# Kernel tuning notes

Measured on AMD Instinct MI355X. Metric: run time of the kernel, lower is better.

The kernel has to match this reference:

```python
import jax, jax.numpy as jnp
import numpy as np

B, P, D = 64, 128, 128   # clouds, points per cloud, vec_dim
N = B * P                # 8192 nodes
EPS = 1e-5


def _complete_graph_edges():
    # knn_graph with k == total node count => complete graph per cloud (no self loops)
    i = np.arange(P)
    ii, jj = np.meshgrid(i, i, indexing='ij')
    m = ii != jj
    li, lj = ii[m], jj[m]                      # [P*(P-1)] local pairs
    off = (np.arange(B) * P)[:, None]          # cloud offsets
    src = (off + li[None, :]).reshape(-1)      # neighbor index
    dst = (off + lj[None, :]).reshape(-1)      # center index
    return jnp.asarray(src, jnp.int32), jnp.asarray(dst, jnp.int32)


def setup_inputs() -> dict:
    key = jax.random.key(0)
    ks = jax.random.split(key, 4)
    src, dst = _complete_graph_edges()
    return {
        'x': jax.random.normal(ks[0], (N, D), jnp.float32),
        'xyz': jax.random.normal(ks[1], (N, 3), jnp.float32),
        'W_xyz': jax.random.normal(ks[2], (3, D), jnp.float32) * 0.1,
        'bn_gamma': jnp.ones((D,), jnp.float32),
        'bn_beta': jnp.zeros((D,), jnp.float32),
        'W1': jax.random.normal(ks[3], (D, D), jnp.float32) * 0.05,
        'b1': jnp.zeros((D,), jnp.float32),
        'ln_gamma': jnp.ones((D,), jnp.float32),
        'ln_beta': jnp.zeros((D,), jnp.float32),
        'src': src,
        'dst': dst,
    }


def reference(x, xyz, W_xyz, bn_gamma, bn_beta, W1, b1, ln_gamma, ln_beta, src, dst):
    n = x.shape[0]
    rela_xyz = xyz[src] - xyz[dst]                         # [E, 3]
    rela_x = x[src] - x[dst]                               # [E, D]
    dist = jnp.sqrt(jnp.sum(rela_xyz * rela_xyz, axis=-1))  # [E]
    w = jnp.exp(-dist)[:, None]                            # [E, 1]

    # weighted linear + relu, pool by src (global_add_pool over node index)
    h1 = jax.nn.relu((w * rela_x) @ W1 + b1)               # [E, D]
    p1 = jax.ops.segment_sum(h1, src, num_segments=n)      # [N, D]
    mu = jnp.mean(p1, axis=-1, keepdims=True)
    var = jnp.var(p1, axis=-1, keepdims=True)
    x = x + ((p1 - mu) / jnp.sqrt(var + EPS)) * ln_gamma + ln_beta

    # xyz projection branch, BatchNorm1d (training-mode batch stats)
    h2 = jax.nn.relu(rela_xyz @ W_xyz)                     # [E, D]
    p2 = jax.ops.segment_sum(h2, src, num_segments=n)      # [N, D]
    bmu = jnp.mean(p2, axis=0)
    bvar = jnp.var(p2, axis=0)
    x = x + ((p2 - bmu) / jnp.sqrt(bvar + EPS)) * bn_gamma + bn_beta
    return x
```

## Files before the change

kernel.cpp:

```cpp
#include <hip/hip_runtime.h>
#include <stdint.h>

#define EPS 1e-5f
#define N_NODES 8192

typedef __attribute__((ext_vector_type(8))) short short8;
typedef __attribute__((ext_vector_type(4))) float floatx4;
typedef __attribute__((ext_vector_type(2))) float floatx2;

__device__ __forceinline__ unsigned short f2bf(float f) {
    uint32_t u = __float_as_uint(f);
    u += 0x7FFFu + ((u >> 16) & 1u);
    return (unsigned short)(u >> 16);
}

__global__ __launch_bounds__(256, 4) void fused_gemm_p2_kernel(
    const float* __restrict__ x, const float* __restrict__ xyz,
    const float* __restrict__ W_xyz, const float* __restrict__ W1,
    float* __restrict__ y_ws, float* __restrict__ p2_ws, float* __restrict__ stat_ws)
{
    __shared__ __align__(16) unsigned char s_mem[128 * 136 * 2];
    const int tid = threadIdx.x;

    if (blockIdx.x < 128) {
        unsigned short* s_w1t = (unsigned short*)s_mem;

        {
            const int n = tid >> 1;
            const int kh = (tid & 1) * 64;
            unsigned short* row = s_w1t + n * 136 + kh;
#pragma unroll
            for (int j = 0; j < 32; ++j) {
                float a = W1[(kh + 2 * j) * 128 + n];
                float b = W1[(kh + 2 * j + 1) * 128 + n];
                uint32_t pk = (uint32_t)f2bf(a) | ((uint32_t)f2bf(b) << 16);
                *(uint32_t*)(row + 2 * j) = pk;
            }
        }

        const int w = tid >> 6, lane = tid & 63;
        const int ml = lane & 15, q = lane >> 4;
        const int rbw = blockIdx.x * 64 + w * 16;

        short8 afrag[4];
#pragma unroll
        for (int c = 0; c < 4; ++c) {
            const float* px = x + (rbw + ml) * 128 + c * 32 + q * 8;
            floatx4 v0 = *(const floatx4*)px;
            floatx4 v1 = *(const floatx4*)(px + 4);
            short8 a;
            a[0] = (short)f2bf(v0[0]); a[1] = (short)f2bf(v0[1]);
            a[2] = (short)f2bf(v0[2]); a[3] = (short)f2bf(v0[3]);
            a[4] = (short)f2bf(v1[0]); a[5] = (short)f2bf(v1[1]);
            a[6] = (short)f2bf(v1[2]); a[7] = (short)f2bf(v1[3]);
            afrag[c] = a;
        }
        __syncthreads();

#pragma unroll
        for (int nt = 0; nt < 8; ++nt) {
            floatx4 acc = {0.f, 0.f, 0.f, 0.f};
            const int ncol = nt * 16 + ml;
#pragma unroll
            for (int c = 0; c < 4; ++c) {
                short8 b = *(const short8*)(s_w1t + ncol * 136 + c * 32 + q * 8);
                acc = __builtin_amdgcn_mfma_f32_16x16x32_bf16(afrag[c], b, acc, 0, 0, 0);
            }
#pragma unroll
            for (int r = 0; r < 4; ++r)
                y_ws[(rbw + q * 4 + r) * 128 + ncol] = acc[r];
        }
    } else {
        float* s_xyz = (float*)s_mem;
        float* s_red = (float*)(s_mem + 2048);

        const int bb = blockIdx.x - 128;
        const int c = bb >> 3, s = bb & 7;
        const int d = tid & 127, h = tid >> 7;
        const int node0 = c * 128, i0 = s * 16;

        if (tid < 128) {
            const float* p = xyz + (node0 + tid) * 3;
            s_xyz[tid * 4 + 0] = p[0];
            s_xyz[tid * 4 + 1] = p[1];
            s_xyz[tid * 4 + 2] = p[2];
            s_xyz[tid * 4 + 3] = 0.f;
        }
        __syncthreads();

        const float w0 = W_xyz[d], w1c = W_xyz[128 + d], w2c = W_xyz[256 + d];
        const floatx2 zv2 = {0.f, 0.f};
        floatx2 zi[8], a2[8];
#pragma unroll
        for (int r = 0; r < 16; ++r) {
            const int ia = i0 + r;
            zi[r >> 1][r & 1] = s_xyz[ia * 4] * w0 + s_xyz[ia * 4 + 1] * w1c
                              + s_xyz[ia * 4 + 2] * w2c;
            a2[r >> 1][r & 1] = 0.f;
        }
        const float* xp = s_xyz + h * 256;
#pragma unroll 4
        for (int j = 0; j < 64; ++j) {
            floatx4 xj = *(const floatx4*)(xp + j * 4);
            const float zj = xj[0] * w0 + xj[1] * w1c + xj[2] * w2c;
            const floatx2 zj2 = {zj, zj};
#pragma unroll
            for (int r = 0; r < 8; ++r)
                a2[r] += __builtin_elementwise_max(zi[r] - zj2, zv2);
        }
        if (h == 1) {
#pragma unroll
            for (int r = 0; r < 16; ++r) s_red[r * 128 + d] = a2[r >> 1][r & 1];
        }
        __syncthreads();
        if (h == 0) {
            float bs = 0.f, bq = 0.f;
#pragma unroll
            for (int r = 0; r < 16; ++r) {
                const float v2 = a2[r >> 1][r & 1] + s_red[r * 128 + d];
                p2_ws[(node0 + i0 + r) * 128 + d] = v2;
                bs += v2;
                bq += v2 * v2;
            }
            const int bank = (bb & 3) * 256;
            atomicAdd(stat_ws + bank + d,       bs);
            atomicAdd(stat_ws + bank + 128 + d, bq);
        }
    }
}

__global__ __launch_bounds__(256, 4) void cloud_main_kernel(
    const float* __restrict__ x, const float* __restrict__ xyz,
    const float* __restrict__ b1, const float* __restrict__ ln_gamma,
    const float* __restrict__ ln_beta, const float* __restrict__ bn_gamma,
    const float* __restrict__ bn_beta, const float* __restrict__ y_ws,
    const float* __restrict__ p2_ws, const float* __restrict__ stat_ws,
    float* __restrict__ out)
{
    __shared__ float s_xyz[512];
    __shared__ float s_w[1024];
    __shared__ float s_red[1024];
    __shared__ float s_p1[1088];
    __shared__ float s_mu[8];
    __shared__ float s_rs[8];
    __shared__ float s_A[128];
    __shared__ float s_B[128];

    const int bx = blockIdx.x;
    const int c = bx & 63, s = bx >> 6;
    const int tid = threadIdx.x;
    const int d = tid & 127, h = tid >> 7;
    const int node0 = c * 128;
    const int i0 = s * 8;

    if (tid < 128) {
        const float* p = xyz + (node0 + tid) * 3;
        s_xyz[tid * 4 + 0] = p[0];
        s_xyz[tid * 4 + 1] = p[1];
        s_xyz[tid * 4 + 2] = p[2];
        s_xyz[tid * 4 + 3] = 0.f;
        float sm = 0.f, sq = 0.f;
#pragma unroll
        for (int b = 0; b < 4; ++b) {
            sm += stat_ws[b * 256 + tid];
            sq += stat_ws[b * 256 + 128 + tid];
        }
        const float mu = sm * (1.f / 8192.f);
        const float var = sq * (1.f / 8192.f) - mu * mu;
        const float A = rsqrtf(var + EPS) * bn_gamma[tid];
        s_A[tid] = A;
        s_B[tid] = bn_beta[tid] - mu * A;
    }
    __syncthreads();

    for (int e = tid; e < 1024; e += 256) {
        const int j = e >> 3, ii = e & 7, ia = i0 + ii;
        float dx = s_xyz[ia * 4]     - s_xyz[j * 4];
        float dy = s_xyz[ia * 4 + 1] - s_xyz[j * 4 + 1];
        float dz = s_xyz[ia * 4 + 2] - s_xyz[j * 4 + 2];
        s_w[j * 8 + ii] = __expf(-sqrtf(dx * dx + dy * dy + dz * dz));
    }
    __syncthreads();

    const float b1d = b1[d];
    const floatx2 b1v = {b1d, b1d};
    const floatx2 zv2 = {0.f, 0.f};

    floatx2 yi[4], a1[4];
#pragma unroll
    for (int r = 0; r < 8; ++r) {
        yi[r >> 1][r & 1] = y_ws[(node0 + i0 + r) * 128 + d];
        a1[r >> 1][r & 1] = 0.f;
    }

    const float* yrow = y_ws + (node0 + h * 64) * 128 + d;
    const float* wp = s_w + h * 512;

#pragma unroll 4
    for (int j = 0; j < 64; ++j) {
        const float yj = yrow[j * 128];
        floatx4 wa = *(const floatx4*)(wp + j * 8);
        floatx4 wb = *(const floatx4*)(wp + j * 8 + 4);
        const floatx2 yj2 = {yj, yj};
        floatx2 wlo = {wa[0], wa[1]}, wmd = {wa[2], wa[3]};
        floatx2 wh0 = {wb[0], wb[1]}, wh1 = {wb[2], wb[3]};
        a1[0] += __builtin_elementwise_max(wlo * (yi[0] - yj2) + b1v, zv2);
        a1[1] += __builtin_elementwise_max(wmd * (yi[1] - yj2) + b1v, zv2);
        a1[2] += __builtin_elementwise_max(wh0 * (yi[2] - yj2) + b1v, zv2);
        a1[3] += __builtin_elementwise_max(wh1 * (yi[3] - yj2) + b1v, zv2);
    }

    if (h == 1) {
#pragma unroll
        for (int r = 0; r < 8; ++r) s_red[r * 128 + d] = a1[r >> 1][r & 1];
    }
    __syncthreads();

    if (h == 0) {
        const float selfc = fmaxf(b1d, 0.f);
#pragma unroll
        for (int r = 0; r < 8; ++r) {
            const float v1 = a1[r >> 1][r & 1] + s_red[r * 128 + d] - selfc;
            a1[r >> 1][r & 1] = v1;
            s_p1[r * 136 + d] = v1;
        }
    }
    __syncthreads();

    {
        const int ii = tid >> 5, sub = tid & 31;
        floatx4 v = *(const floatx4*)(s_p1 + ii * 136 + sub * 4);
        float ps = v[0] + v[1] + v[2] + v[3];
        float pq = v[0] * v[0] + v[1] * v[1] + v[2] * v[2] + v[3] * v[3];
#pragma unroll
        for (int m = 1; m < 32; m <<= 1) {
            ps += __shfl_xor(ps, m, 64);
            pq += __shfl_xor(pq, m, 64);
        }
        if (sub == 0) {
            const float mu = ps * (1.f / 128.f);
            const float var = pq * (1.f / 128.f) - mu * mu;
            s_mu[ii] = mu;
            s_rs[ii] = rsqrtf(var + EPS);
        }
    }
    __syncthreads();

    if (h == 0) {
        const float lng = ln_gamma[d], lnb = ln_beta[d];
        const float A = s_A[d], B = s_B[d];
#pragma unroll
        for (int r = 0; r < 8; ++r) {
            const int gi = node0 + i0 + r;
            out[gi * 128 + d] = x[gi * 128 + d]
                + (a1[r >> 1][r & 1] - s_mu[r]) * s_rs[r] * lng + lnb
                + p2_ws[gi * 128 + d] * A + B;
        }
    }
}

extern "C" void kernel_launch(void* const* d_in, const int* in_sizes, int n_in,
                              void* d_out, int out_size, void* d_ws, size_t ws_size,
                              hipStream_t stream) {
    const float* x        = (const float*)d_in[0];
    const float* xyz      = (const float*)d_in[1];
    const float* W_xyz    = (const float*)d_in[2];
    const float* bn_gamma = (const float*)d_in[3];
    const float* bn_beta  = (const float*)d_in[4];
    const float* W1       = (const float*)d_in[5];
    const float* b1       = (const float*)d_in[6];
    const float* ln_gamma = (const float*)d_in[7];
    const float* ln_beta  = (const float*)d_in[8];
    float* out = (float*)d_out;

    float* y_ws    = (float*)d_ws;
    float* p2_ws   = y_ws + N_NODES * 128;
    float* stat_ws = p2_ws + N_NODES * 128;

    hipMemsetAsync(stat_ws, 0, 1024 * sizeof(float), stream);
    fused_gemm_p2_kernel<<<640, 256, 0, stream>>>(x, xyz, W_xyz, W1, y_ws, p2_ws, stat_ws);
    cloud_main_kernel<<<1024, 256, 0, stream>>>(x, xyz, b1, ln_gamma, ln_beta,
                                                bn_gamma, bn_beta, y_ws, p2_ws,
                                                stat_ws, out);
}
```

Baseline: 110.5 us.

## Merge two kernels into one persistent launch with atomic-counter grid sync

Combines the GEMM/p2 kernel and the cloud main kernel into a single 1024-block launch. Blocks 0-127 compute y and bump one counter, blocks 128-639 compute p2 and batch stats and bump a second counter. Every block then runs the per-cloud phase, spin-waiting on the counters only at the points where y and the BN stats are needed. The goal is to remove the second kernel launch and its boundary, and to overlap the edge-weight setup with producer work. The spin-waits depend on all producer blocks being resident or scheduled before the consumers that wait on them, which risks deadlock or stalls if blocks do not all fit at once.

```diff
diff --git a/kernel.cpp b/kernel.cpp
--- a/kernel.cpp
+++ b/kernel.cpp
@@ -14,17 +14,22 @@
     return (unsigned short)(u >> 16);
 }
 
-__global__ __launch_bounds__(256, 4) void fused_gemm_p2_kernel(
+__global__ __launch_bounds__(256, 4) void fused_all_kernel(
     const float* __restrict__ x, const float* __restrict__ xyz,
     const float* __restrict__ W_xyz, const float* __restrict__ W1,
-    float* __restrict__ y_ws, float* __restrict__ p2_ws, float* __restrict__ stat_ws)
+    const float* __restrict__ b1, const float* __restrict__ ln_gamma,
+    const float* __restrict__ ln_beta, const float* __restrict__ bn_gamma,
+    const float* __restrict__ bn_beta, float* __restrict__ y_ws,
+    float* __restrict__ p2_ws, float* __restrict__ stat_ws,
+    float* __restrict__ out)
 {
-    __shared__ __align__(16) unsigned char s_mem[128 * 136 * 2];
+    __shared__ __align__(16) unsigned char s_mem[34816];
     const int tid = threadIdx.x;
-
-    if (blockIdx.x < 128) {
+    const int bx = blockIdx.x;
+    int* ctrs = (int*)(stat_ws + 1024);
+
+    if (bx < 128) {
         unsigned short* s_w1t = (unsigned short*)s_mem;
-
         {
             const int n = tid >> 1;
             const int kh = (tid & 1) * 64;
@@ -32,20 +37,19 @@
 #pragma unroll
             for (int j = 0; j < 32; ++j) {
                 float a = W1[(kh + 2 * j) * 128 + n];
-                float b = W1[(kh + 2 * j + 1) * 128 + n];
-                uint32_t pk = (uint32_t)f2bf(a) | ((uint32_t)f2bf(b) << 16);
+                float bb = W1[(kh + 2 * j + 1) * 128 + n];
+                uint32_t pk = (uint32_t)f2bf(a) | ((uint32_t)f2bf(bb) << 16);
                 *(uint32_t*)(row + 2 * j) = pk;
             }
         }
-
         const int w = tid >> 6, lane = tid & 63;
         const int ml = lane & 15, q = lane >> 4;
-        const int rbw = blockIdx.x * 64 + w * 16;
+        const int rbw = bx * 64 + w * 16;
 
         short8 afrag[4];
 #pragma unroll
-        for (int c = 0; c < 4; ++c) {
-            const float* px = x + (rbw + ml) * 128 + c * 32 + q * 8;
+        for (int c0 = 0; c0 < 4; ++c0) {
+            const float* px = x + (rbw + ml) * 128 + c0 * 32 + q * 8;
             floatx4 v0 = *(const floatx4*)px;
             floatx4 v1 = *(const floatx4*)(px + 4);
             short8 a;
@@ -53,38 +57,39 @@
             a[2] = (short)f2bf(v0[2]); a[3] = (short)f2bf(v0[3]);
             a[4] = (short)f2bf(v1[0]); a[5] = (short)f2bf(v1[1]);
             a[6] = (short)f2bf(v1[2]); a[7] = (short)f2bf(v1[3]);
-            afrag[c] = a;
-        }
-        __syncthreads();
-
+            afrag[c0] = a;
+        }
+        __syncthreads();
 #pragma unroll
         for (int nt = 0; nt < 8; ++nt) {
             floatx4 acc = {0.f, 0.f, 0.f, 0.f};
             const int ncol = nt * 16 + ml;
 #pragma unroll
-            for (int c = 0; c < 4; ++c) {
-                short8 b = *(const short8*)(s_w1t + ncol * 136 + c * 32 + q * 8);
-                acc = __builtin_amdgcn_mfma_f32_16x16x32_bf16(afrag[c], b, acc, 0, 0, 0);
+            for (int c0 = 0; c0 < 4; ++c0) {
+                short8 bfr = *(const short8*)(s_w1t + ncol * 136 + c0 * 32 + q * 8);
+                acc = __builtin_amdgcn_mfma_f32_16x16x32_bf16(afrag[c0], bfr, acc, 0, 0, 0);
             }
 #pragma unroll
             for (int r = 0; r < 4; ++r)
                 y_ws[(rbw + q * 4 + r) * 128 + ncol] = acc[r];
         }
-    } else {
-        float* s_xyz = (float*)s_mem;
-        float* s_red = (float*)(s_mem + 2048);
-
-        const int bb = blockIdx.x - 128;
+        __syncthreads();
+        if (tid == 0)
+            __hip_atomic_fetch_add(&ctrs[0], 1, __ATOMIC_RELEASE, __HIP_MEMORY_SCOPE_AGENT);
+    } else if (bx < 640) {
+        float* s_xyzp = (float*)s_mem;
+        float* s_redp = (float*)(s_mem + 2048);
+        const int bb = bx - 128;
         const int c = bb >> 3, s = bb & 7;
         const int d = tid & 127, h = tid >> 7;
         const int node0 = c * 128, i0 = s * 16;
 
         if (tid < 128) {
             const float* p = xyz + (node0 + tid) * 3;
-            s_xyz[tid * 4 + 0] = p[0];
-            s_xyz[tid * 4 + 1] = p[1];
-            s_xyz[tid * 4 + 2] = p[2];
-            s_xyz[tid * 4 + 3] = 0.f;
+            s_xyzp[tid * 4 + 0] = p[0];
+            s_xyzp[tid * 4 + 1] = p[1];
+            s_xyzp[tid * 4 + 2] = p[2];
+            s_xyzp[tid * 4 + 3] = 0.f;
         }
         __syncthreads();
 
@@ -94,11 +99,11 @@
 #pragma unroll
         for (int r = 0; r < 16; ++r) {
             const int ia = i0 + r;
-            zi[r >> 1][r & 1] = s_xyz[ia * 4] * w0 + s_xyz[ia * 4 + 1] * w1c
-                              + s_xyz[ia * 4 + 2] * w2c;
+            zi[r >> 1][r & 1] = s_xyzp[ia * 4] * w0 + s_xyzp[ia * 4 + 1] * w1c
+                              + s_xyzp[ia * 4 + 2] * w2c;
             a2[r >> 1][r & 1] = 0.f;
         }
-        const float* xp = s_xyz + h * 256;
+        const float* xp = s_xyzp + h * 256;
 #pragma unroll 4
         for (int j = 0; j < 64; ++j) {
             floatx4 xj = *(const floatx4*)(xp + j * 4);
@@ -110,14 +115,14 @@
         }
         if (h == 1) {
 #pragma unroll
-            for (int r = 0; r < 16; ++r) s_red[r * 128 + d] = a2[r >> 1][r & 1];
+            for (int r = 0; r < 16; ++r) s_redp[r * 128 + d] = a2[r >> 1][r & 1];
         }
         __syncthreads();
         if (h == 0) {
             float bs = 0.f, bq = 0.f;
 #pragma unroll
             for (int r = 0; r < 16; ++r) {
-                const float v2 = a2[r >> 1][r & 1] + s_red[r * 128 + d];
+                const float v2 = a2[r >> 1][r & 1] + s_redp[r * 128 + d];
                 p2_ws[(node0 + i0 + r) * 128 + d] = v2;
                 bs += v2;
                 bq += v2 * v2;
@@ -126,29 +131,22 @@
             atomicAdd(stat_ws + bank + d,       bs);
             atomicAdd(stat_ws + bank + 128 + d, bq);
         }
-    }
-}
-
-__global__ __launch_bounds__(256, 4) void cloud_main_kernel(
-    const float* __restrict__ x, const float* __restrict__ xyz,
-    const float* __restrict__ b1, const float* __restrict__ ln_gamma,
-    const float* __restrict__ ln_beta, const float* __restrict__ bn_gamma,
-    const float* __restrict__ bn_beta, const float* __restrict__ y_ws,
-    const float* __restrict__ p2_ws, const float* __restrict__ stat_ws,
-    float* __restrict__ out)
-{
-    __shared__ float s_xyz[512];
-    __shared__ float s_w[1024];
-    __shared__ float s_red[1024];
-    __shared__ float s_p1[1088];
-    __shared__ float s_mu[8];
-    __shared__ float s_rs[8];
-    __shared__ float s_A[128];
-    __shared__ float s_B[128];
-
-    const int bx = blockIdx.x;
+        __syncthreads();
+        if (tid == 0)
+            __hip_atomic_fetch_add(&ctrs[1], 1, __ATOMIC_RELEASE, __HIP_MEMORY_SCOPE_AGENT);
+    }
+
+    __syncthreads();
+    float* s_xyz = (float*)s_mem;
+    float* s_w   = (float*)(s_mem + 2048);
+    float* s_red = (float*)(s_mem + 6144);
+    float* s_p1  = (float*)(s_mem + 10240);
+    float* s_mu  = (float*)(s_mem + 14592);
+    float* s_rs  = (float*)(s_mem + 14656);
+    float* s_A   = (float*)(s_mem + 14720);
+    float* s_B   = (float*)(s_mem + 15232);
+
     const int c = bx & 63, s = bx >> 6;
-    const int tid = threadIdx.x;
     const int d = tid & 127, h = tid >> 7;
     const int node0 = c * 128;
     const int i0 = s * 8;
@@ -159,17 +157,6 @@
         s_xyz[tid * 4 + 1] = p[1];
         s_xyz[tid * 4 + 2] = p[2];
         s_xyz[tid * 4 + 3] = 0.f;
-        float sm = 0.f, sq = 0.f;
-#pragma unroll
-        for (int b = 0; b < 4; ++b) {
-            sm += stat_ws[b * 256 + tid];
-            sq += stat_ws[b * 256 + 128 + tid];
-        }
-        const float mu = sm * (1.f / 8192.f);
-        const float var = sq * (1.f / 8192.f) - mu * mu;
-        const float A = rsqrtf(var + EPS) * bn_gamma[tid];
-        s_A[tid] = A;
-        s_B[tid] = bn_beta[tid] - mu * A;
     }
     __syncthreads();
 
@@ -180,6 +167,10 @@
         float dz = s_xyz[ia * 4 + 2] - s_xyz[j * 4 + 2];
         s_w[j * 8 + ii] = __expf(-sqrtf(dx * dx + dy * dy + dz * dz));
     }
+
+    while (__hip_atomic_load(&ctrs[0], __ATOMIC_RELAXED, __HIP_MEMORY_SCOPE_AGENT) < 128)
+        __builtin_amdgcn_s_sleep(16);
+    (void)__hip_atomic_load(&ctrs[0], __ATOMIC_ACQUIRE, __HIP_MEMORY_SCOPE_AGENT);
     __syncthreads();
 
     const float b1d = b1[d];
@@ -243,6 +234,23 @@
             s_mu[ii] = mu;
             s_rs[ii] = rsqrtf(var + EPS);
         }
+    }
+
+    while (__hip_atomic_load(&ctrs[1], __ATOMIC_RELAXED, __HIP_MEMORY_SCOPE_AGENT) < 512)
+        __builtin_amdgcn_s_sleep(16);
+    (void)__hip_atomic_load(&ctrs[1], __ATOMIC_ACQUIRE, __HIP_MEMORY_SCOPE_AGENT);
+    if (tid < 128) {
+        float sm = 0.f, sq = 0.f;
+#pragma unroll
+        for (int b = 0; b < 4; ++b) {
+            sm += stat_ws[b * 256 + tid];
+            sq += stat_ws[b * 256 + 128 + tid];
+        }
+        const float mu = sm * (1.f / 8192.f);
+        const float var = sq * (1.f / 8192.f) - mu * mu;
+        const float A = rsqrtf(var + EPS) * bn_gamma[tid];
+        s_A[tid] = A;
+        s_B[tid] = bn_beta[tid] - mu * A;
     }
     __syncthreads();
 
@@ -277,9 +285,8 @@
     float* p2_ws   = y_ws + N_NODES * 128;
     float* stat_ws = p2_ws + N_NODES * 128;
 
-    hipMemsetAsync(stat_ws, 0, 1024 * sizeof(float), stream);
-    fused_gemm_p2_kernel<<<640, 256, 0, stream>>>(x, xyz, W_xyz, W1, y_ws, p2_ws, stat_ws);
-    cloud_main_kernel<<<1024, 256, 0, stream>>>(x, xyz, b1, ln_gamma, ln_beta,
-                                                bn_gamma, bn_beta, y_ws, p2_ws,
-                                                stat_ws, out);
+    hipMemsetAsync(stat_ws, 0, 1032 * sizeof(float), stream);
+    fused_all_kernel<<<1024, 256, 0, stream>>>(x, xyz, W_xyz, W1, b1,
+                                               ln_gamma, ln_beta, bn_gamma, bn_beta,
+                                               y_ws, p2_ws, stat_ws, out);
 }
```

Result: slower. 208.3 us (+88.5%).
